# Optimization experiments

Measured on AMD Instinct MI355X. Metric: run time of the kernel, lower is better.

Reference implementation:

```python
import jax, jax.numpy as jnp
import numpy as np

# ---- static configuration matching init_kwargs ----
SEG = 2                 # segment_size hard-coded in the module
MUL0, MUL1 = 256, 128   # irreps = 256x0e + 128x1o
G = MUL1 // SEG         # 64 groups of 2x1o
INV_DIM = MUL0 + 3 * G  # 448 scalars (0e) after concat with channel_mix
N_IRREPS = INV_DIM + MUL1 + G + 3 * G  # 832 total irreps after regroup
N_NODES = 32768
EPS = 1e-6
_ISQ2 = 1.0 / np.sqrt(2.0)
_ISQ3 = 1.0 / np.sqrt(3.0)
_ISQ6 = 1.0 / np.sqrt(6.0)


def _cg_l2(a, b):
    """CG contraction 1 x 1 -> 2: project a_i b_j onto the 5 orthonormal
    symmetric-traceless basis matrices. a, b: [..., 3] -> [..., 5]."""
    ax, ay, az = a[..., 0], a[..., 1], a[..., 2]
    bx, by, bz = b[..., 0], b[..., 1], b[..., 2]
    return jnp.stack([
        (ax * by + ay * bx) * _ISQ2,
        (ax * bz + az * bx) * _ISQ2,
        (ay * bz + az * by) * _ISQ2,
        (ax * bx - ay * by) * _ISQ2,
        (2 * az * bz - ax * bx - ay * by) * _ISQ6,
    ], axis=-1)


def setup_inputs() -> dict:
    key = jax.random.key(0)
    k = jax.random.split(key, 5)
    return {
        "x":   jax.random.normal(k[0], (N_NODES, MUL0 + 3 * MUL1), dtype=jnp.float32),
        "W1":  jax.random.normal(k[1], (INV_DIM, INV_DIM),   dtype=jnp.float32),
        "W2":  jax.random.normal(k[2], (INV_DIM, N_IRREPS),  dtype=jnp.float32),
        "Wl0": jax.random.normal(k[3], (INV_DIM, MUL0),      dtype=jnp.float32),
        "Wl1": jax.random.normal(k[4], (MUL1, MUL1),         dtype=jnp.float32),
    }


def reference(x, W1, W2, Wl0, Wl1):
    N = x.shape[0]
    dt = x.dtype
    s = x[:, :MUL0]                       # [N, 256]  0e features
    v = x[:, MUL0:].reshape(N, MUL1, 3)   # [N, 128, 3]  1o features

    # ---- segmented tensor_square: groups of 2x1o -> 3x0e + 1x1e + 3x2e ----
    vg = v.reshape(N, G, SEG, 3)
    a, b = vg[:, :, 0], vg[:, :, 1]
    sq2 = jnp.sqrt(jnp.asarray(2.0, dt))
    # 0e: symmetric pairs (0,0), (0,1)*sqrt2, (1,1); CG = delta_ij/sqrt3
    t0 = jnp.stack([(a * a).sum(-1), sq2 * (a * b).sum(-1), (b * b).sum(-1)], -1) * _ISQ3  # [N,G,3]
    # 1e: antisymmetric pair (0,1); CG = eps/sqrt2, pair factor sqrt2 -> plain cross
    t1 = jnp.cross(a, b)                                                                   # [N,G,3]
    # 2e: symmetric pairs
    t2 = jnp.stack([_cg_l2(a, a), sq2 * _cg_l2(a, b), _cg_l2(b, b)], 2)                    # [N,G,3,5]

    # ---- concatenate + regroup (axis_to_mul folds group axis into mul) ----
    s_all = jnp.concatenate([s, t0.reshape(N, 3 * G)], -1)  # [N,448]  448x0e
    v1o = v                                                 # [N,128,3] 128x1o
    v1e = t1                                                # [N,64,3]   64x1e
    v2e = t2.reshape(N, 3 * G, 5)                           # [N,192,5] 192x2e

    # ---- gating MLP on invariants: [448 -> 448 (silu) -> 832] ----
    inv_fan = jnp.sqrt(jnp.asarray(INV_DIM, dt))
    h = jax.nn.silu(s_all @ W1 / inv_fan)
    gates = h @ W2 / inv_fan                                # [N, 832] one scalar per irrep
    g0, g1o, g1e, g2e = jnp.split(gates, [INV_DIM, INV_DIM + MUL1, INV_DIM + MUL1 + G], -1)
    s_all = s_all * g0
    v1o = v1o * g1o[..., None]
    # (v1e * g1e, v2e * g2e are dropped by the Linear below -> omitted, output identical)
    del v1e, v2e, g1e, g2e

    # ---- e3nn Linear to output irreps 256x0e + 128x1o (1e, 2e have no output) ----
    o0 = s_all @ Wl0 / inv_fan                                                   # [N,256]
    o1 = jnp.einsum('nmi,mk->nki', v1o, Wl1) / jnp.sqrt(jnp.asarray(MUL1, dt))   # [N,128,3]

    # ---- equivariant layer norm ----
    mu = o0.mean(-1, keepdims=True)
    var = ((o0 - mu) ** 2).mean(-1, keepdims=True)
    o0 = (o0 - mu) * jax.lax.rsqrt(var + EPS)
    rms = jnp.sqrt((o1 ** 2).mean((-2, -1), keepdims=True) + EPS)
    o1 = o1 / rms

    return jnp.concatenate([o0, o1.reshape(N, 3 * MUL1)], -1)  # [N, 640]
```

## Files before the change

kernel.cpp:

```cpp
#include <hip/hip_runtime.h>
#include <math.h>


typedef float floatx4 __attribute__((ext_vector_type(4)));
typedef __bf16 bf16x8 __attribute__((ext_vector_type(8)));

__device__ __forceinline__ unsigned short f2bf(float f) {
    __bf16 h = (__bf16)f;
    return __builtin_bit_cast(unsigned short, h);
}
__device__ __forceinline__ float bf2f(unsigned short u) {
    union { unsigned u; float f; } v; v.u = ((unsigned)u) << 16; return v.f;
}

__global__ __launch_bounds__(256) void wcast_kernel(
    const float* __restrict__ W1, const float* __restrict__ W2,
    const float* __restrict__ Wl0, const float* __restrict__ Wl1,
    unsigned short* __restrict__ W1F, unsigned short* __restrict__ W2F,
    unsigned short* __restrict__ Wl0F, unsigned short* __restrict__ Wl1F)
{
    int idx = blockIdx.x * 256 + threadIdx.x;
    const float* src; unsigned short* dst;
    int NKC, ld, colTrue, k, rem;
    if (idx < 28672) {
        k = idx / 64; rem = idx % 64; src = W1; dst = W1F; NKC = 14; ld = 448; colTrue = 448;
    } else if (idx < 64512) {
        int r = idx - 28672;
        k = r / 80; rem = r % 80; src = W2; dst = W2F; NKC = 14; ld = 832; colTrue = 576;
    } else if (idx < 78848) {
        int r = idx - 64512;
        k = r / 32; rem = r % 32; src = Wl0; dst = Wl0F; NKC = 14; ld = 256; colTrue = 256;
    } else if (idx < 80896) {
        int r = idx - 78848;
        k = r / 16; rem = r % 16; src = Wl1; dst = Wl1F; NKC = 4; ld = 128; colTrue = 128;
    } else return;
    int t = rem >> 1, c8 = rem & 1;
    int col0 = t * 16 + c8 * 8;
    float v[8] = {0.f, 0.f, 0.f, 0.f, 0.f, 0.f, 0.f, 0.f};
    if (col0 < colTrue) {
        const float* s = src + (size_t)k * ld + col0;
        float4 f0 = *(const float4*)s;
        float4 f1 = *(const float4*)(s + 4);
        v[0]=f0.x; v[1]=f0.y; v[2]=f0.z; v[3]=f0.w;
        v[4]=f1.x; v[5]=f1.y; v[6]=f1.z; v[7]=f1.w;
    }
    int kc = k >> 5, q = (k >> 3) & 3, e = k & 7;
    unsigned short* base = dst + ((size_t)(t * NKC + kc) * 64 + q * 16 + c8 * 8) * 8 + e;
    #pragma unroll
    for (int d = 0; d < 8; ++d) base[d * 8] = f2bf(v[d]);
}

template<int MT, int NT, int NKC>
__device__ __forceinline__ void gemm_stream(
    const unsigned short* __restrict__ BF,
    const unsigned short* __restrict__ Albs, const int ldsA, const int rowBase,
    const int lane, const int l15, const int quad, const int wn,
    floatx4 (&acc)[MT][NT])
{
    const unsigned short* bp[NT];
    #pragma unroll
    for (int j = 0; j < NT; ++j)
        bp[j] = BF + ((size_t)(wn + 8 * j) * NKC * 64 + lane) * 8;
    #pragma unroll
    for (int kc = 0; kc < NKC; ++kc) {
        bf16x8 af[MT];
        #pragma unroll
        for (int mt = 0; mt < MT; ++mt)
            af[mt] = *(const bf16x8*)&Albs[(rowBase + mt * 16 + l15) * ldsA + kc * 32 + quad * 8];
        #pragma unroll
        for (int j = 0; j < NT; ++j) {
            bf16x8 bfv = *(const bf16x8*)(bp[j] + kc * 512);
            #pragma unroll
            for (int mt = 0; mt < MT; ++mt)
                acc[mt][j] = __builtin_amdgcn_mfma_f32_16x16x32_bf16(af[mt], bfv, acc[mt][j], 0, 0, 0);
        }
    }
}

__global__ __launch_bounds__(512, 2) void fused_kernel(
    const float* __restrict__ x,
    const unsigned short* __restrict__ W1F,
    const unsigned short* __restrict__ W2F,
    const unsigned short* __restrict__ Wl0F,
    const unsigned short* __restrict__ Wl1F,
    float* __restrict__ out)
{
    __shared__ unsigned short sa[64][472];
    __shared__ unsigned short hb[64][472];
    __shared__ unsigned short g1[64][128];
    __shared__ float red[1600];

    const int tid  = threadIdx.x;
    const int lane = tid & 63;
    const int l15  = lane & 15;
    const int quad = lane >> 4;
    const int wn   = tid >> 6;
    const int n0   = blockIdx.x * 64;

    const float s1 = 0.047245559f;
    const float s2 = 0.088388348f;

    {
        const int r = tid >> 3, sub = tid & 7;
        const float* xr = x + (size_t)(n0 + r) * 640;
        #pragma unroll
        for (int i = 0; i < 8; ++i) {
            int c4 = i * 8 + sub;
            float4 f = *(const float4*)(xr + c4 * 4);
            unsigned short* o = &sa[r][c4 * 4];
            o[0] = f2bf(f.x); o[1] = f2bf(f.y); o[2] = f2bf(f.z); o[3] = f2bf(f.w);
        }
        const float* xv = xr + 256;
        #pragma unroll
        for (int i = 0; i < 8; ++i) {
            int g = i * 8 + sub;
            const float2* vg = (const float2*)(xv + 6 * g);
            float2 p0 = vg[0], p1 = vg[1], p2 = vg[2];
            float ax = p0.x, ay = p0.y, az = p1.x;
            float bx = p1.y, by = p2.x, bz = p2.y;
            float aa = ax*ax + ay*ay + az*az;
            float ab = ax*bx + ay*by + az*bz;
            float bb = bx*bx + by*by + bz*bz;
            const float ISQ3 = 0.57735026918962576f;
            const float SQ2  = 1.41421356237309505f;
            sa[r][256 + 3*g]     = f2bf(aa * ISQ3);
            sa[r][256 + 3*g + 1] = f2bf(SQ2 * ab * ISQ3);
            sa[r][256 + 3*g + 2] = f2bf(bb * ISQ3);
        }
    }
    __syncthreads();

    {
        floatx4 acc[4][4] = {};
        gemm_stream<4,4,14>(W1F, &sa[0][0], 472, 0, lane, l15, quad, wn, acc);
        #pragma unroll
        for (int j = 0; j < 4; ++j) {
            const int colb = (wn + 8*j) * 16;
            if (colb < 448) {
                const int col = colb + l15;
                #pragma unroll
                for (int mt = 0; mt < 4; ++mt)
                    #pragma unroll
                    for (int r = 0; r < 4; ++r) {
                        float v = acc[mt][j][r] * s1;
                        v = v / (1.f + __expf(-v));
                        hb[mt*16 + quad*4 + r][col] = f2bf(v);
                    }
            }
        }
    }
    __syncthreads();

    {
        floatx4 acc[4][5] = {};
        gemm_stream<4,5,14>(W2F, &hb[0][0], 472, 0, lane, l15, quad, wn, acc);
        __syncthreads();
        #pragma unroll
        for (int j = 0; j < 5; ++j) {
            const int colb = (wn + 8*j) * 16;
            if (colb < 448) {
                const int col = colb + l15;
                #pragma unroll
                for (int mt = 0; mt < 4; ++mt)
                    #pragma unroll
                    for (int r = 0; r < 4; ++r) {
                        const int row = mt*16 + quad*4 + r;
                        hb[row][col] = f2bf(bf2f(sa[row][col]) * (acc[mt][j][r] * s1));
                    }
            } else if (colb < 576) {
                const int m = colb - 448 + l15;
                #pragma unroll
                for (int mt = 0; mt < 4; ++mt)
                    #pragma unroll
                    for (int r = 0; r < 4; ++r) {
                        const int row = mt*16 + quad*4 + r;
                        g1[row][m] = f2bf(acc[mt][j][r] * s1);
                    }
            }
        }
    }
    __syncthreads();

    {
        unsigned short* wmp = &sa[0][0];
        #pragma unroll
        for (int e0 = 0; e0 < 6144; e0 += 512) {
            int e4 = e0 + tid;
            int rl = e4 / 96;
            int c4 = (e4 - rl * 96) * 4;
            float4 xv = *(const float4*)(x + (size_t)(n0 + rl) * 640 + 256 + c4);
            float vv[4] = {xv.x, xv.y, xv.z, xv.w};
            #pragma unroll
            for (int d = 0; d < 4; ++d) {
                int rem = c4 + d;
                int m = rem / 3;
                int i = rem - 3 * m;
                wmp[(rl * 3 + i) * 136 + m] = f2bf(vv[d] * bf2f(g1[rl][m]));
            }
        }
    }
    __syncthreads();

    {
        floatx4 acc[4][2] = {};
        gemm_stream<4,2,14>(Wl0F, &hb[0][0], 472, 0, lane, l15, quad, wn, acc);
        #pragma unroll
        for (int mt = 0; mt < 4; ++mt)
            #pragma unroll
            for (int r = 0; r < 4; ++r) {
                float sv = 0.f, sq = 0.f;
                #pragma unroll
                for (int j = 0; j < 2; ++j) {
                    float v = acc[mt][j][r] * s1;
                    sv += v; sq += v * v;
                }
                #pragma unroll
                for (int off = 1; off <= 8; off <<= 1) {
                    sv += __shfl_xor(sv, off);
                    sq += __shfl_xor(sq, off);
                }
                if (l15 == 0) {
                    const int row = mt*16 + quad*4 + r;
                    red[row * 8 + wn]       = sv;
                    red[512 + row * 8 + wn] = sq;
                }
            }
        __syncthreads();
        #pragma unroll
        for (int mt = 0; mt < 4; ++mt)
            #pragma unroll
            for (int r = 0; r < 4; ++r) {
                const int row = mt*16 + quad*4 + r;
                float ts = 0.f, tq = 0.f;
                #pragma unroll
                for (int w2 = 0; w2 < 8; ++w2) {
                    ts += red[row*8 + w2];
                    tq += red[512 + row*8 + w2];
                }
                float mu  = ts * (1.f/256.f);
                float var = tq * (1.f/256.f) - mu * mu;
                float rln = rsqrtf(var + 1e-6f);
                float* orow = out + (size_t)(n0 + row) * 640;
                #pragma unroll
                for (int j = 0; j < 2; ++j)
                    orow[(wn + 8*j)*16 + l15] = (acc[mt][j][r] * s1 - mu) * rln;
            }
    }
    __syncthreads();

    {
        floatx4 acc[12][1] = {};
        gemm_stream<12,1,4>(Wl1F, &sa[0][0] , 136, 0, lane, l15, quad, wn, acc);
        #pragma unroll
        for (int mt = 0; mt < 12; ++mt)
            #pragma unroll
            for (int r = 0; r < 4; ++r) {
                float v = acc[mt][0][r] * s2;
                float q = v * v;
                #pragma unroll
                for (int off = 1; off <= 8; off <<= 1) q += __shfl_xor(q, off);
                if (l15 == 0) {
                    const int row = mt*16 + quad*4 + r;
                    red[row * 8 + wn] = q;
                }
            }
        __syncthreads();
        if (tid < 64) {
            float s = 0.f;
            #pragma unroll
            for (int rr = 0; rr < 3; ++rr)
                #pragma unroll
                for (int w2 = 0; w2 < 8; ++w2)
                    s += red[(tid*3 + rr) * 8 + w2];
            red[1536 + tid] = rsqrtf(s * (1.f/384.f) + 1e-6f);
        }
        __syncthreads();
        #pragma unroll
        for (int mt = 0; mt < 12; ++mt)
            #pragma unroll
            for (int r = 0; r < 4; ++r) {
                const int row = mt*16 + quad*4 + r;
                const int nl  = row / 3;
                const int i   = row - 3 * nl;
                const float rms = red[1536 + nl];
                float* op = out + (size_t)(n0 + nl) * 640 + 256 + i;
                op[3 * (wn*16 + l15)] = acc[mt][0][r] * s2 * rms;
            }
    }
}

extern "C" void kernel_launch(void* const* d_in, const int* in_sizes, int n_in,
                              void* d_out, int out_size, void* d_ws, size_t ws_size,
                              hipStream_t stream) {
    const float* x   = (const float*)d_in[0];
    const float* W1  = (const float*)d_in[1];
    const float* W2  = (const float*)d_in[2];
    const float* Wl0 = (const float*)d_in[3];
    const float* Wl1 = (const float*)d_in[4];
    float* out = (float*)d_out;
    char* ws = (char*)d_ws;

    unsigned short* W1F  = (unsigned short*)(ws + 0);
    unsigned short* W2F  = (unsigned short*)(ws + 458752);
    unsigned short* Wl0F = (unsigned short*)(ws + 1032192);
    unsigned short* Wl1F = (unsigned short*)(ws + 1261568);

    wcast_kernel<<<dim3(316), dim3(256), 0, stream>>>(W1, W2, Wl0, Wl1, W1F, W2F, Wl0F, Wl1F);
    fused_kernel<<<dim3(512), dim3(512), 0, stream>>>(x, W1F, W2F, Wl0F, Wl1F, out);
}
```

Baseline: 248.3 us.

## Halve node tile to 32 rows per block and rewrite weight-cast kernel

```diff
diff --git a/kernel.cpp b/kernel.cpp
--- a/kernel.cpp
+++ b/kernel.cpp
@@ -21,33 +21,24 @@
 {
     int idx = blockIdx.x * 256 + threadIdx.x;
     const float* src; unsigned short* dst;
-    int NKC, ld, colTrue, k, rem;
+    int NKC, ld, colTrue, r;
     if (idx < 28672) {
-        k = idx / 64; rem = idx % 64; src = W1; dst = W1F; NKC = 14; ld = 448; colTrue = 448;
+        r = idx; src = W1; dst = W1F; NKC = 14; ld = 448; colTrue = 448;
     } else if (idx < 64512) {
-        int r = idx - 28672;
-        k = r / 80; rem = r % 80; src = W2; dst = W2F; NKC = 14; ld = 832; colTrue = 576;
+        r = idx - 28672; src = W2; dst = W2F; NKC = 14; ld = 832; colTrue = 576;
     } else if (idx < 78848) {
-        int r = idx - 64512;
-        k = r / 32; rem = r % 32; src = Wl0; dst = Wl0F; NKC = 14; ld = 256; colTrue = 256;
+        r = idx - 64512; src = Wl0; dst = Wl0F; NKC = 14; ld = 256; colTrue = 256;
     } else if (idx < 80896) {
-        int r = idx - 78848;
-        k = r / 16; rem = r % 16; src = Wl1; dst = Wl1F; NKC = 4; ld = 128; colTrue = 128;
+        r = idx - 78848; src = Wl1; dst = Wl1F; NKC = 4; ld = 128; colTrue = 128;
     } else return;
-    int t = rem >> 1, c8 = rem & 1;
-    int col0 = t * 16 + c8 * 8;
-    float v[8] = {0.f, 0.f, 0.f, 0.f, 0.f, 0.f, 0.f, 0.f};
-    if (col0 < colTrue) {
-        const float* s = src + (size_t)k * ld + col0;
-        float4 f0 = *(const float4*)s;
-        float4 f1 = *(const float4*)(s + 4);
-        v[0]=f0.x; v[1]=f0.y; v[2]=f0.z; v[3]=f0.w;
-        v[4]=f1.x; v[5]=f1.y; v[6]=f1.z; v[7]=f1.w;
-    }
-    int kc = k >> 5, q = (k >> 3) & 3, e = k & 7;
-    unsigned short* base = dst + ((size_t)(t * NKC + kc) * 64 + q * 16 + c8 * 8) * 8 + e;
+    int lane = r & 63, kc = (r >> 6) % NKC, t = (r >> 6) / NKC;
+    int col = t * 16 + (lane & 15);
+    int k0  = kc * 32 + (lane >> 4) * 8;
+    unsigned short v[8];
     #pragma unroll
-    for (int d = 0; d < 8; ++d) base[d * 8] = f2bf(v[d]);
+    for (int e = 0; e < 8; ++e)
+        v[e] = (col < colTrue) ? f2bf(src[(size_t)(k0 + e) * ld + col]) : (unsigned short)0;
+    *(uint4*)(dst + (size_t)r * 8) = *(const uint4*)v;
 }
 
 template<int MT, int NT, int NKC>
@@ -77,7 +68,7 @@
     }
 }
 
-__global__ __launch_bounds__(512, 2) void fused_kernel(
+__global__ __launch_bounds__(512, 4) void fused_kernel(
     const float* __restrict__ x,
     const unsigned short* __restrict__ W1F,
     const unsigned short* __restrict__ W2F,
@@ -85,35 +76,37 @@
     const unsigned short* __restrict__ Wl1F,
     float* __restrict__ out)
 {
-    __shared__ unsigned short sa[64][472];
-    __shared__ unsigned short hb[64][472];
-    __shared__ unsigned short g1[64][128];
-    __shared__ float red[1600];
+    __shared__ unsigned short sa[32][472];
+    __shared__ unsigned short hb[32][472];
+    __shared__ unsigned short g1[32][128];
+    __shared__ float red[800];
 
     const int tid  = threadIdx.x;
     const int lane = tid & 63;
     const int l15  = lane & 15;
     const int quad = lane >> 4;
     const int wn   = tid >> 6;
-    const int n0   = blockIdx.x * 64;
+    const int n0   = blockIdx.x * 32;
 
     const float s1 = 0.047245559f;
     const float s2 = 0.088388348f;
 
     {
-        const int r = tid >> 3, sub = tid & 7;
+        const int r = tid >> 4, sub = tid & 15;
         const float* xr = x + (size_t)(n0 + r) * 640;
         #pragma unroll
-        for (int i = 0; i < 8; ++i) {
-            int c4 = i * 8 + sub;
+        for (int i = 0; i < 4; ++i) {
+            int c4 = i * 16 + sub;
             float4 f = *(const float4*)(xr + c4 * 4);
-            unsigned short* o = &sa[r][c4 * 4];
-            o[0] = f2bf(f.x); o[1] = f2bf(f.y); o[2] = f2bf(f.z); o[3] = f2bf(f.w);
+            uint2 p;
+            p.x = (unsigned)f2bf(f.x) | ((unsigned)f2bf(f.y) << 16);
+            p.y = (unsigned)f2bf(f.z) | ((unsigned)f2bf(f.w) << 16);
+            *(uint2*)&sa[r][c4 * 4] = p;
         }
         const float* xv = xr + 256;
         #pragma unroll
-        for (int i = 0; i < 8; ++i) {
-            int g = i * 8 + sub;
+        for (int i = 0; i < 4; ++i) {
+            int g = i * 16 + sub;
             const float2* vg = (const float2*)(xv + 6 * g);
             float2 p0 = vg[0], p1 = vg[1], p2 = vg[2];
             float ax = p0.x, ay = p0.y, az = p1.x;
@@ -131,15 +124,15 @@
     __syncthreads();
 
     {
-        floatx4 acc[4][4] = {};
-        gemm_stream<4,4,14>(W1F, &sa[0][0], 472, 0, lane, l15, quad, wn, acc);
+        floatx4 acc[2][4] = {};
+        gemm_stream<2,4,14>(W1F, &sa[0][0], 472, 0, lane, l15, quad, wn, acc);
         #pragma unroll
         for (int j = 0; j < 4; ++j) {
             const int colb = (wn + 8*j) * 16;
             if (colb < 448) {
                 const int col = colb + l15;
                 #pragma unroll
-                for (int mt = 0; mt < 4; ++mt)
+                for (int mt = 0; mt < 2; ++mt)
                     #pragma unroll
                     for (int r = 0; r < 4; ++r) {
                         float v = acc[mt][j][r] * s1;
@@ -152,8 +145,8 @@
     __syncthreads();
 
     {
-        floatx4 acc[4][5] = {};
-        gemm_stream<4,5,14>(W2F, &hb[0][0], 472, 0, lane, l15, quad, wn, acc);
+        floatx4 acc[2][5] = {};
+        gemm_stream<2,5,14>(W2F, &hb[0][0], 472, 0, lane, l15, quad, wn, acc);
         __syncthreads();
         #pragma unroll
         for (int j = 0; j < 5; ++j) {
@@ -161,7 +154,7 @@
             if (colb < 448) {
                 const int col = colb + l15;
                 #pragma unroll
-                for (int mt = 0; mt < 4; ++mt)
+                for (int mt = 0; mt < 2; ++mt)
                     #pragma unroll
                     for (int r = 0; r < 4; ++r) {
                         const int row = mt*16 + quad*4 + r;
@@ -170,7 +163,7 @@
             } else if (colb < 576) {
                 const int m = colb - 448 + l15;
                 #pragma unroll
-                for (int mt = 0; mt < 4; ++mt)
+                for (int mt = 0; mt < 2; ++mt)
                     #pragma unroll
                     for (int r = 0; r < 4; ++r) {
                         const int row = mt*16 + quad*4 + r;
@@ -184,7 +177,7 @@
     {
         unsigned short* wmp = &sa[0][0];
         #pragma unroll
-        for (int e0 = 0; e0 < 6144; e0 += 512) {
+        for (int e0 = 0; e0 < 3072; e0 += 512) {
             int e4 = e0 + tid;
             int rl = e4 / 96;
             int c4 = (e4 - rl * 96) * 4;
@@ -202,10 +195,10 @@
     __syncthreads();
 
     {
-        floatx4 acc[4][2] = {};
-        gemm_stream<4,2,14>(Wl0F, &hb[0][0], 472, 0, lane, l15, quad, wn, acc);
-        #pragma unroll
-        for (int mt = 0; mt < 4; ++mt)
+        floatx4 acc[2][2] = {};
+        gemm_stream<2,2,14>(Wl0F, &hb[0][0], 472, 0, lane, l15, quad, wn, acc);
+        #pragma unroll
+        for (int mt = 0; mt < 2; ++mt)
             #pragma unroll
             for (int r = 0; r < 4; ++r) {
                 float sv = 0.f, sq = 0.f;
@@ -222,12 +215,12 @@
                 if (l15 == 0) {
                     const int row = mt*16 + quad*4 + r;
                     red[row * 8 + wn]       = sv;
-                    red[512 + row * 8 + wn] = sq;
+                    red[256 + row * 8 + wn] = sq;
                 }
             }
         __syncthreads();
         #pragma unroll
-        for (int mt = 0; mt < 4; ++mt)
+        for (int mt = 0; mt < 2; ++mt)
             #pragma unroll
             for (int r = 0; r < 4; ++r) {
                 const int row = mt*16 + quad*4 + r;
@@ -235,7 +228,7 @@
                 #pragma unroll
                 for (int w2 = 0; w2 < 8; ++w2) {
                     ts += red[row*8 + w2];
-                    tq += red[512 + row*8 + w2];
+                    tq += red[256 + row*8 + w2];
                 }
                 float mu  = ts * (1.f/256.f);
                 float var = tq * (1.f/256.f) - mu * mu;
@@ -249,10 +242,10 @@
     __syncthreads();
 
     {
-        floatx4 acc[12][1] = {};
-        gemm_stream<12,1,4>(Wl1F, &sa[0][0] , 136, 0, lane, l15, quad, wn, acc);
-        #pragma unroll
-        for (int mt = 0; mt < 12; ++mt)
+        floatx4 acc[6][1] = {};
+        gemm_stream<6,1,4>(Wl1F, &sa[0][0] , 136, 0, lane, l15, quad, wn, acc);
+        #pragma unroll
+        for (int mt = 0; mt < 6; ++mt)
             #pragma unroll
             for (int r = 0; r < 4; ++r) {
                 float v = acc[mt][0][r] * s2;
@@ -265,24 +258,24 @@
                 }
             }
         __syncthreads();
-        if (tid < 64) {
+        if (tid < 32) {
             float s = 0.f;
             #pragma unroll
             for (int rr = 0; rr < 3; ++rr)
                 #pragma unroll
                 for (int w2 = 0; w2 < 8; ++w2)
                     s += red[(tid*3 + rr) * 8 + w2];
-            red[1536 + tid] = rsqrtf(s * (1.f/384.f) + 1e-6f);
+            red[768 + tid] = rsqrtf(s * (1.f/384.f) + 1e-6f);
         }
         __syncthreads();
         #pragma unroll
-        for (int mt = 0; mt < 12; ++mt)
+        for (int mt = 0; mt < 6; ++mt)
             #pragma unroll
             for (int r = 0; r < 4; ++r) {
                 const int row = mt*16 + quad*4 + r;
                 const int nl  = row / 3;
                 const int i   = row - 3 * nl;
-                const float rms = red[1536 + nl];
+                const float rms = red[768 + nl];
                 float* op = out + (size_t)(n0 + nl) * 640 + 256 + i;
                 op[3 * (wn*16 + l15)] = acc[mt][0][r] * s2 * rms;
             }
@@ -306,5 +299,5 @@
     unsigned short* Wl1F = (unsigned short*)(ws + 1261568);
 
     wcast_kernel<<<dim3(316), dim3(256), 0, stream>>>(W1, W2, Wl0, Wl1, W1F, W2F, Wl0F, Wl1F);
-    fused_kernel<<<dim3(512), dim3(512), 0, stream>>>(x, W1F, W2F, Wl0F, Wl1F, out);
-}
+    fused_kernel<<<dim3(1024), dim3(512), 0, stream>>>(x, W1F, W2F, Wl0F, Wl1F, out);
+}
```

New measurement: 249.5 us. About the same (+0.5%).
